# Optimization experiments

Hardware: AMD Instinct MI355X
Metric: run time of the kernel (lower is better)

The kernel has to match this reference:

```python
import jax, jax.numpy as jnp
import numpy as np

N_NODES = 200000
D_IN = 512
HID = 512
D_OUT = 256
B = 1024
SIZES = (25, 10)


def setup_inputs() -> dict:
    key = jax.random.key(0)
    ks = jax.random.split(key, 8)
    x = jax.random.normal(ks[0], (N_NODES, D_IN), dtype=jnp.float32)
    nodes = jax.random.randint(ks[1], (B,), 0, N_NODES)
    neigh1 = jax.random.randint(ks[2], (B * SIZES[0],), 0, N_NODES)
    neigh2 = jax.random.randint(ks[3], (B * SIZES[0] * SIZES[1],), 0, N_NODES)
    # SAGEAggregator weights, stored as [in, out] (torch Linear weight transposed); bias=False
    s = 0.05
    Ws0 = jax.random.normal(ks[4], (D_IN, HID), dtype=jnp.float32) * s
    Wn0 = jax.random.normal(ks[5], (D_IN, HID), dtype=jnp.float32) * s
    Ws1 = jax.random.normal(ks[6], (2 * HID, D_OUT), dtype=jnp.float32) * s
    Wn1 = jax.random.normal(ks[7], (2 * HID, D_OUT), dtype=jnp.float32) * s
    return {"x": x, "nodes": nodes, "neigh1": neigh1, "neigh2": neigh2,
            "Ws0": Ws0, "Wn0": Wn0, "Ws1": Ws1, "Wn1": Wn1}


def _sage_agg(h_self, h_neigh, Ws, Wn, concat):
    # h_self: [M, d], h_neigh: [M, fanout, d] -> mean aggregate then linear transforms
    m = jnp.mean(h_neigh, axis=1)
    a = h_self @ Ws
    b = m @ Wn
    return jnp.concatenate([a, b], axis=-1) if concat else a + b


def reference(x, nodes, neigh1, neigh2, Ws0, Wn0, Ws1, Wn1):
    # gather features for root nodes and sampled 1-hop / 2-hop neighborhoods
    h0 = x[nodes]    # [B, D_IN]
    h1 = x[neigh1]   # [B*25, D_IN]
    h2 = x[neigh2]   # [B*25*10, D_IN]
    d = D_IN
    # layer 0 (concat=True), act=relu, dropout is identity (inference)
    h0 = jax.nn.relu(_sage_agg(h0, h1.reshape(-1, SIZES[0], d), Ws0, Wn0, True))  # [B, 2*HID]
    h1 = jax.nn.relu(_sage_agg(h1, h2.reshape(-1, SIZES[1], d), Ws0, Wn0, True))  # [B*25, 2*HID]
    d2 = 2 * HID
    # layer 1 (last aggregator, concat=False -> sum), no activation
    out = _sage_agg(h0, h1.reshape(-1, SIZES[0], d2), Ws1, Wn1, False)  # [B, D_OUT]
    return out
```

## Files before the change

### kernel.cpp

```cpp
#include <hip/hip_runtime.h>
#include <hip/hip_bf16.h>


#define DEVINL __device__ __forceinline__

typedef __bf16 bf16x8 __attribute__((ext_vector_type(8)));
typedef float f32x4 __attribute__((ext_vector_type(4)));

DEVINL unsigned short f2bf(float f) {
  union { float f; unsigned u; } v; v.f = f;
  unsigned r = v.u + 0x7FFFu + ((v.u >> 16) & 1u);
  return (unsigned short)(r >> 16);
}
DEVINL float bf2f(unsigned short h) {
  union { unsigned u; float f; } v; v.u = ((unsigned)h) << 16;
  return v.f;
}

DEVINL void gload_lds16(const void* g, void* l) {
  __builtin_amdgcn_global_load_lds(
      (const __attribute__((address_space(1))) void*)g,
      (__attribute__((address_space(3))) void*)l, 16, 0, 0);
}

__global__ void weights_cast_kernel(const float* __restrict__ Ws0, const float* __restrict__ Wn0,
                                    const float* __restrict__ Ws1, const float* __restrict__ Wn1,
                                    unsigned short* __restrict__ WT0s, unsigned short* __restrict__ WT0n,
                                    unsigned short* __restrict__ WT1s, unsigned short* __restrict__ WT1n) {
  int t = blockIdx.x * 256 + threadIdx.x;
  int region = t >> 18, local = t & 262143;
  const float* W; unsigned short* WT; int k, n, N;
  if (region == 0)      { W = Ws0; WT = WT0s; }
  else if (region == 1) { W = Wn0; WT = WT0n; }
  else if (region == 2) { W = Ws1; WT = WT1s; }
  else                  { W = Wn1; WT = WT1n; }
  if (region < 2) { k = local & 511;  n = local >> 9;  N = 512; }
  else            { k = local & 1023; n = local >> 10; N = 256; }
  WT[local] = f2bf(W[(size_t)k * N + n]);
}

__global__ void zero_out_kernel(float4* __restrict__ out) {
  out[blockIdx.x * 256 + threadIdx.x] = float4{0.f, 0.f, 0.f, 0.f};
}

__global__ void gather_self_kernel(const float* __restrict__ x,
                                   const int* __restrict__ neigh1,
                                   const int* __restrict__ nodes,
                                   unsigned short* __restrict__ out) {
  int row = blockIdx.x * 2 + (threadIdx.x >> 7);
  int src = row < 25600 ? neigh1[row] : nodes[row - 25600];
  int c4 = (threadIdx.x & 127) << 2;
  const float4 v = *reinterpret_cast<const float4*>(x + (size_t)src * 512 + c4);
  ushort4 o; o.x = f2bf(v.x); o.y = f2bf(v.y); o.z = f2bf(v.z); o.w = f2bf(v.w);
  *reinterpret_cast<ushort4*>(out + (size_t)row * 512 + c4) = o;
}

__global__ void gather_mean10_kernel(const float* __restrict__ x,
                                     const int* __restrict__ idx,
                                     unsigned short* __restrict__ out) {
  int row = blockIdx.x * 2 + (threadIdx.x >> 7);
  int c4 = (threadIdx.x & 127) << 2;
  float4 acc = {0.f, 0.f, 0.f, 0.f};
  const int* ip = idx + (size_t)row * 10;
  #pragma unroll
  for (int j = 0; j < 10; ++j) {
    const float4 v = *reinterpret_cast<const float4*>(x + (size_t)ip[j] * 512 + c4);
    acc.x += v.x; acc.y += v.y; acc.z += v.z; acc.w += v.w;
  }
  const float s = 0.1f;
  ushort4 o; o.x = f2bf(acc.x * s); o.y = f2bf(acc.y * s);
  o.z = f2bf(acc.z * s); o.w = f2bf(acc.w * s);
  *reinterpret_cast<ushort4*>(out + (size_t)row * 512 + c4) = o;
}

template <int COLS>
__global__ void group_mean25_kernel(const unsigned short* __restrict__ in,
                                    unsigned short* __restrict__ out) {
  constexpr int TPG = COLS / 4;
  int g = blockIdx.x * (256 / TPG) + threadIdx.x / TPG;
  int c4 = (threadIdx.x % TPG) * 4;
  float a0 = 0, a1 = 0, a2 = 0, a3 = 0;
  for (int j = 0; j < 25; ++j) {
    ushort4 v = *reinterpret_cast<const ushort4*>(in + ((size_t)g * 25 + j) * COLS + c4);
    a0 += bf2f(v.x); a1 += bf2f(v.y); a2 += bf2f(v.z); a3 += bf2f(v.w);
  }
  const float s = 1.0f / 25.0f;
  ushort4 o; o.x = f2bf(a0 * s); o.y = f2bf(a1 * s); o.z = f2bf(a2 * s); o.w = f2bf(a3 * s);
  *reinterpret_cast<ushort4*>(out + (size_t)g * COLS + c4) = o;
}

template <bool RELU, bool OUTF32, bool ATOMIC>
DEVINL void gemm_core(const unsigned short* __restrict__ A, int lda,
                      const unsigned short* __restrict__ Bt, int ldb,
                      void* __restrict__ C, int ldc, int Kc,
                      long tm, long tn, long col0,
                      unsigned short* As, unsigned short* Bs) {
  const int t = threadIdx.x;
  const int w = t >> 6;
  const int l = t & 63;
  const int wm = w >> 1, wn = w & 1;
  f32x4 acc[4][4] = {};
  const int s_r = l >> 2;
  const int s_kc = (l & 3) * 8;

  for (int kt = 0; kt < Kc; kt += 32) {
    __syncthreads();
    #pragma unroll
    for (int r = 0; r < 2; ++r) {
      const int chunk = r * 64 + w * 16;
      gload_lds16(A + (size_t)(tm + chunk + s_r) * lda + kt + s_kc, As + chunk * 32);
      gload_lds16(Bt + (size_t)(tn + chunk + s_r) * ldb + kt + s_kc, Bs + chunk * 32);
    }
    __syncthreads();

    bf16x8 af[4], bfr[4];
    const unsigned short* Ab = As + ((size_t)(wm * 64 + (l & 15)) * 32 + (l >> 4) * 8);
    const unsigned short* Bb = Bs + ((size_t)(wn * 64 + (l & 15)) * 32 + (l >> 4) * 8);
    #pragma unroll
    for (int f = 0; f < 4; ++f) {
      af[f] = *reinterpret_cast<const bf16x8*>(Ab + f * 16 * 32);
      bfr[f] = *reinterpret_cast<const bf16x8*>(Bb + f * 16 * 32);
    }
    #pragma unroll
    for (int i = 0; i < 4; ++i)
      #pragma unroll
      for (int j = 0; j < 4; ++j)
        acc[i][j] = __builtin_amdgcn_mfma_f32_16x16x32_bf16(af[i], bfr[j], acc[i][j], 0, 0, 0);
  }

  #pragma unroll
  for (int i = 0; i < 4; ++i) {
    #pragma unroll
    for (int j = 0; j < 4; ++j) {
      #pragma unroll
      for (int r = 0; r < 4; ++r) {
        float v = acc[i][j][r];
        if (RELU) v = fmaxf(v, 0.0f);
        const long row = tm + wm * 64 + i * 16 + (l >> 4) * 4 + r;
        const long col = col0 + tn + wn * 64 + j * 16 + (l & 15);
        if (OUTF32) {
          if (ATOMIC) atomicAdd((float*)C + row * ldc + col, v);
          else        ((float*)C)[row * ldc + col] = v;
        } else {
          ((unsigned short*)C)[row * ldc + col] = f2bf(v);
        }
      }
    }
  }
}

__global__ __launch_bounds__(256) void gemm0_kernel(
    const unsigned short* __restrict__ Hall, const unsigned short* __restrict__ Hmall,
    const unsigned short* __restrict__ WT0s, const unsigned short* __restrict__ WT0n,
    unsigned short* __restrict__ C1all) {
  __shared__ __align__(16) unsigned short As[128 * 32];
  __shared__ __align__(16) unsigned short Bs[128 * 32];
  const int half = blockIdx.x >> 2;
  const long tn = (long)(blockIdx.x & 3) * 128;
  const long tm = (long)blockIdx.y * 128;
  gemm_core<true, false, false>(half ? Hmall : Hall, 512,
                                half ? WT0n : WT0s, 512,
                                C1all, 1024, 512, tm, tn, half ? 512 : 0, As, Bs);
}

__global__ __launch_bounds__(256) void gemm1_kernel(
    const unsigned short* __restrict__ C0, const unsigned short* __restrict__ WT1s,
    const unsigned short* __restrict__ M1, const unsigned short* __restrict__ WT1n,
    float* __restrict__ out) {
  __shared__ __align__(16) unsigned short As[128 * 32];
  __shared__ __align__(16) unsigned short Bs[128 * 32];
  const int pass = blockIdx.z >> 2;
  const int k0 = (blockIdx.z & 3) * 256;
  gemm_core<false, true, true>((pass ? M1 : C0) + k0, 1024,
                               (pass ? WT1n : WT1s) + k0, 1024,
                               out, 256, 256,
                               (long)blockIdx.y * 128, (long)blockIdx.x * 128, 0, As, Bs);
}

extern "C" void kernel_launch(void* const* d_in, const int* in_sizes, int n_in,
                              void* d_out, int out_size, void* d_ws, size_t ws_size,
                              hipStream_t stream) {
  const float* x      = (const float*)d_in[0];
  const int*   nodes  = (const int*)d_in[1];
  const int*   neigh1 = (const int*)d_in[2];
  const int*   neigh2 = (const int*)d_in[3];
  const float* Ws0    = (const float*)d_in[4];
  const float* Wn0    = (const float*)d_in[5];
  const float* Ws1    = (const float*)d_in[6];
  const float* Wn1    = (const float*)d_in[7];
  float* out = (float*)d_out;

  char* p = (char*)d_ws;
  unsigned short* WT0s  = (unsigned short*)p; p += (size_t)512 * 512 * 2;
  unsigned short* WT0n  = (unsigned short*)p; p += (size_t)512 * 512 * 2;
  unsigned short* WT1s  = (unsigned short*)p; p += (size_t)256 * 1024 * 2;
  unsigned short* WT1n  = (unsigned short*)p; p += (size_t)256 * 1024 * 2;
  unsigned short* Hall  = (unsigned short*)p; p += (size_t)26624 * 512 * 2;
  unsigned short* Hmall = (unsigned short*)p; p += (size_t)26624 * 512 * 2;
  unsigned short* C1all = (unsigned short*)p; p += (size_t)26624 * 1024 * 2;
  unsigned short* M1    = (unsigned short*)p; p += (size_t)1024 * 1024 * 2;

  unsigned short* H0m = Hmall + (size_t)25600 * 512;
  const unsigned short* C0 = C1all + (size_t)25600 * 1024;

  hipLaunchKernelGGL(weights_cast_kernel, dim3(4096), dim3(256), 0, stream,
                     Ws0, Wn0, Ws1, Wn1, WT0s, WT0n, WT1s, WT1n);
  hipLaunchKernelGGL(zero_out_kernel, dim3(256), dim3(256), 0, stream, (float4*)out);

  hipLaunchKernelGGL(gather_self_kernel, dim3(13312), dim3(256), 0, stream, x, neigh1, nodes, Hall);
  hipLaunchKernelGGL(gather_mean10_kernel, dim3(12800), dim3(256), 0, stream, x, neigh2, Hmall);
  hipLaunchKernelGGL(group_mean25_kernel<512>, dim3(512), dim3(256), 0, stream, Hall, H0m);

  hipLaunchKernelGGL(gemm0_kernel, dim3(8, 208), dim3(256), 0, stream,
                     Hall, Hmall, WT0s, WT0n, C1all);

  hipLaunchKernelGGL(group_mean25_kernel<1024>, dim3(1024), dim3(256), 0, stream, C1all, M1);

  hipLaunchKernelGGL(gemm1_kernel, dim3(2, 8, 8), dim3(256), 0, stream,
                     C0, WT1s, M1, WT1n, out);
}
```

Before: 190.9 us.

## Fuse group-mean into GEMM0 epilogue with atomics and merge kernels into phases

Replaces the materialized 26624x1024 bf16 C1all buffer with an epilogue that sums ReLU outputs of each 25-row group and accumulates them into an fp32 M1 buffer via atomics. Only the root-node rows are stored as bf16. The separate gather, cast, zero and mean kernels are merged into phase kernels, so the self-half GEMM overlaps with the 2-hop gather. The aim is to cut a large intermediate write and re-read plus several launches. In exchange it adds many global float atomics, an extra fp32 scratch buffer and a conversion pass, and the fp32 summation order becomes nondeterministic.

```diff
diff --git a/kernel.cpp b/kernel.cpp
--- a/kernel.cpp
+++ b/kernel.cpp
@@ -23,77 +23,12 @@
       (__attribute__((address_space(3))) void*)l, 16, 0, 0);
 }
 
-__global__ void weights_cast_kernel(const float* __restrict__ Ws0, const float* __restrict__ Wn0,
-                                    const float* __restrict__ Ws1, const float* __restrict__ Wn1,
-                                    unsigned short* __restrict__ WT0s, unsigned short* __restrict__ WT0n,
-                                    unsigned short* __restrict__ WT1s, unsigned short* __restrict__ WT1n) {
-  int t = blockIdx.x * 256 + threadIdx.x;
-  int region = t >> 18, local = t & 262143;
-  const float* W; unsigned short* WT; int k, n, N;
-  if (region == 0)      { W = Ws0; WT = WT0s; }
-  else if (region == 1) { W = Wn0; WT = WT0n; }
-  else if (region == 2) { W = Ws1; WT = WT1s; }
-  else                  { W = Wn1; WT = WT1n; }
-  if (region < 2) { k = local & 511;  n = local >> 9;  N = 512; }
-  else            { k = local & 1023; n = local >> 10; N = 256; }
-  WT[local] = f2bf(W[(size_t)k * N + n]);
-}
-
-__global__ void zero_out_kernel(float4* __restrict__ out) {
-  out[blockIdx.x * 256 + threadIdx.x] = float4{0.f, 0.f, 0.f, 0.f};
-}
-
-__global__ void gather_self_kernel(const float* __restrict__ x,
-                                   const int* __restrict__ neigh1,
-                                   const int* __restrict__ nodes,
-                                   unsigned short* __restrict__ out) {
-  int row = blockIdx.x * 2 + (threadIdx.x >> 7);
-  int src = row < 25600 ? neigh1[row] : nodes[row - 25600];
-  int c4 = (threadIdx.x & 127) << 2;
-  const float4 v = *reinterpret_cast<const float4*>(x + (size_t)src * 512 + c4);
-  ushort4 o; o.x = f2bf(v.x); o.y = f2bf(v.y); o.z = f2bf(v.z); o.w = f2bf(v.w);
-  *reinterpret_cast<ushort4*>(out + (size_t)row * 512 + c4) = o;
-}
-
-__global__ void gather_mean10_kernel(const float* __restrict__ x,
-                                     const int* __restrict__ idx,
-                                     unsigned short* __restrict__ out) {
-  int row = blockIdx.x * 2 + (threadIdx.x >> 7);
-  int c4 = (threadIdx.x & 127) << 2;
-  float4 acc = {0.f, 0.f, 0.f, 0.f};
-  const int* ip = idx + (size_t)row * 10;
-  #pragma unroll
-  for (int j = 0; j < 10; ++j) {
-    const float4 v = *reinterpret_cast<const float4*>(x + (size_t)ip[j] * 512 + c4);
-    acc.x += v.x; acc.y += v.y; acc.z += v.z; acc.w += v.w;
-  }
-  const float s = 0.1f;
-  ushort4 o; o.x = f2bf(acc.x * s); o.y = f2bf(acc.y * s);
-  o.z = f2bf(acc.z * s); o.w = f2bf(acc.w * s);
-  *reinterpret_cast<ushort4*>(out + (size_t)row * 512 + c4) = o;
-}
-
-template <int COLS>
-__global__ void group_mean25_kernel(const unsigned short* __restrict__ in,
-                                    unsigned short* __restrict__ out) {
-  constexpr int TPG = COLS / 4;
-  int g = blockIdx.x * (256 / TPG) + threadIdx.x / TPG;
-  int c4 = (threadIdx.x % TPG) * 4;
-  float a0 = 0, a1 = 0, a2 = 0, a3 = 0;
-  for (int j = 0; j < 25; ++j) {
-    ushort4 v = *reinterpret_cast<const ushort4*>(in + ((size_t)g * 25 + j) * COLS + c4);
-    a0 += bf2f(v.x); a1 += bf2f(v.y); a2 += bf2f(v.z); a3 += bf2f(v.w);
-  }
-  const float s = 1.0f / 25.0f;
-  ushort4 o; o.x = f2bf(a0 * s); o.y = f2bf(a1 * s); o.z = f2bf(a2 * s); o.w = f2bf(a3 * s);
-  *reinterpret_cast<ushort4*>(out + (size_t)g * COLS + c4) = o;
-}
-
-template <bool RELU, bool OUTF32, bool ATOMIC>
+template <int EPI>
 DEVINL void gemm_core(const unsigned short* __restrict__ A, int lda,
                       const unsigned short* __restrict__ Bt, int ldb,
-                      void* __restrict__ C, int ldc, int Kc,
-                      long tm, long tn, long col0,
+                      int Kc, long tm, long tn, int col0,
+                      unsigned short* __restrict__ C0, float* __restrict__ M1f,
+                      float* __restrict__ out, int ldc,
                       unsigned short* As, unsigned short* Bs) {
   const int t = threadIdx.x;
   const int w = t >> 6;
@@ -128,42 +63,157 @@
         acc[i][j] = __builtin_amdgcn_mfma_f32_16x16x32_bf16(af[i], bfr[j], acc[i][j], 0, 0, 0);
   }
 
-  #pragma unroll
-  for (int i = 0; i < 4; ++i) {
-    #pragma unroll
-    for (int j = 0; j < 4; ++j) {
-      #pragma unroll
-      for (int r = 0; r < 4; ++r) {
-        float v = acc[i][j][r];
-        if (RELU) v = fmaxf(v, 0.0f);
-        const long row = tm + wm * 64 + i * 16 + (l >> 4) * 4 + r;
-        const long col = col0 + tn + wn * 64 + j * 16 + (l & 15);
-        if (OUTF32) {
-          if (ATOMIC) atomicAdd((float*)C + row * ldc + col, v);
-          else        ((float*)C)[row * ldc + col] = v;
-        } else {
-          ((unsigned short*)C)[row * ldc + col] = f2bf(v);
+  const int q = l >> 4, cl = l & 15;
+  if (EPI == 0) {
+    if (tm < 25600) {
+      #pragma unroll
+      for (int i = 0; i < 4; ++i) {
+        const int base = (int)tm + wm * 64 + i * 16 + q * 4;
+        const int g = base / 25;
+        const int rem = base - g * 25;
+        #pragma unroll
+        for (int j = 0; j < 4; ++j) {
+          const int col = col0 + (int)tn + wn * 64 + j * 16 + cl;
+          float v0 = fmaxf(acc[i][j][0], 0.f), v1 = fmaxf(acc[i][j][1], 0.f);
+          float v2 = fmaxf(acc[i][j][2], 0.f), v3 = fmaxf(acc[i][j][3], 0.f);
+          if (rem <= 21) {
+            atomicAdd(M1f + (size_t)g * 1024 + col, v0 + v1 + v2 + v3);
+          } else {
+            const int s = 25 - rem;
+            float a = v0, b = 0.f;
+            if (s > 1) a += v1; else b += v1;
+            if (s > 2) a += v2; else b += v2;
+            b += v3;
+            atomicAdd(M1f + (size_t)g * 1024 + col, a);
+            atomicAdd(M1f + (size_t)(g + 1) * 1024 + col, b);
+          }
         }
       }
-    }
-  }
-}
-
-__global__ __launch_bounds__(256) void gemm0_kernel(
-    const unsigned short* __restrict__ Hall, const unsigned short* __restrict__ Hmall,
-    const unsigned short* __restrict__ WT0s, const unsigned short* __restrict__ WT0n,
-    unsigned short* __restrict__ C1all) {
+    } else {
+      #pragma unroll
+      for (int i = 0; i < 4; ++i)
+        #pragma unroll
+        for (int j = 0; j < 4; ++j)
+          #pragma unroll
+          for (int r = 0; r < 4; ++r) {
+            const long row = tm - 25600 + wm * 64 + i * 16 + q * 4 + r;
+            const long col = col0 + tn + wn * 64 + j * 16 + cl;
+            C0[row * 1024 + col] = f2bf(fmaxf(acc[i][j][r], 0.f));
+          }
+    }
+  } else {
+    #pragma unroll
+    for (int i = 0; i < 4; ++i)
+      #pragma unroll
+      for (int j = 0; j < 4; ++j)
+        #pragma unroll
+        for (int r = 0; r < 4; ++r) {
+          const long row = tm + wm * 64 + i * 16 + q * 4 + r;
+          const long col = tn + wn * 64 + j * 16 + cl;
+          atomicAdd(out + row * ldc + col, acc[i][j][r]);
+        }
+  }
+}
+
+__global__ __launch_bounds__(256) void phase0_kernel(
+    const float* __restrict__ x, const int* __restrict__ neigh1, const int* __restrict__ nodes,
+    const float* __restrict__ Ws0, const float* __restrict__ Wn0,
+    const float* __restrict__ Ws1, const float* __restrict__ Wn1,
+    unsigned short* __restrict__ Hall,
+    unsigned short* __restrict__ WT0s, unsigned short* __restrict__ WT0n,
+    unsigned short* __restrict__ WT1s, unsigned short* __restrict__ WT1n,
+    float* __restrict__ M1f, float* __restrict__ out) {
+  const int b = blockIdx.x;
+  const int tid = threadIdx.x;
+  if (b < 13312) {
+    int row = b * 2 + (tid >> 7);
+    int src = row < 25600 ? neigh1[row] : nodes[row - 25600];
+    int c4 = (tid & 127) << 2;
+    const float4 v = *reinterpret_cast<const float4*>(x + (size_t)src * 512 + c4);
+    ushort4 o; o.x = f2bf(v.x); o.y = f2bf(v.y); o.z = f2bf(v.z); o.w = f2bf(v.w);
+    *reinterpret_cast<ushort4*>(Hall + (size_t)row * 512 + c4) = o;
+  } else if (b < 13312 + 4096) {
+    int t = (b - 13312) * 256 + tid;
+    int region = t >> 18, local = t & 262143;
+    const float* W; unsigned short* WT;
+    if (region == 0)      { W = Ws0; WT = WT0s; }
+    else if (region == 1) { W = Wn0; WT = WT0n; }
+    else if (region == 2) { W = Ws1; WT = WT1s; }
+    else                  { W = Wn1; WT = WT1n; }
+    int k, n, N;
+    if (region < 2) { k = local & 511;  n = local >> 9;  N = 512; }
+    else            { k = local & 1023; n = local >> 10; N = 256; }
+    WT[local] = f2bf(W[(size_t)k * N + n]);
+  } else if (b < 13312 + 4096 + 1024) {
+    int t = (b - 17408) * 256 + tid;
+    reinterpret_cast<float4*>(M1f)[t] = float4{0.f, 0.f, 0.f, 0.f};
+  } else {
+    int t = (b - 18432) * 256 + tid;
+    reinterpret_cast<float4*>(out)[t] = float4{0.f, 0.f, 0.f, 0.f};
+  }
+}
+
+__global__ __launch_bounds__(256) void phase1_kernel(
+    const float* __restrict__ x, const int* __restrict__ neigh2,
+    const unsigned short* __restrict__ Hall, const unsigned short* __restrict__ WT0s,
+    unsigned short* __restrict__ Hmall,
+    unsigned short* __restrict__ C0, float* __restrict__ M1f) {
   __shared__ __align__(16) unsigned short As[128 * 32];
   __shared__ __align__(16) unsigned short Bs[128 * 32];
-  const int half = blockIdx.x >> 2;
+  const int b = blockIdx.x;
+  const int tid = threadIdx.x;
+  if (b < 832) {
+    const long tm = (long)(b >> 2) * 128;
+    const long tn = (long)(b & 3) * 128;
+    gemm_core<0>(Hall, 512, WT0s, 512, 512, tm, tn, 0, C0, M1f, nullptr, 0, As, Bs);
+  } else if (b < 832 + 12800) {
+    int row = (b - 832) * 2 + (tid >> 7);
+    int c4 = (tid & 127) << 2;
+    float4 acc = {0.f, 0.f, 0.f, 0.f};
+    const int* ip = neigh2 + (size_t)row * 10;
+    #pragma unroll
+    for (int j = 0; j < 10; ++j) {
+      const float4 v = *reinterpret_cast<const float4*>(x + (size_t)ip[j] * 512 + c4);
+      acc.x += v.x; acc.y += v.y; acc.z += v.z; acc.w += v.w;
+    }
+    const float s = 0.1f;
+    ushort4 o; o.x = f2bf(acc.x * s); o.y = f2bf(acc.y * s);
+    o.z = f2bf(acc.z * s); o.w = f2bf(acc.w * s);
+    *reinterpret_cast<ushort4*>(Hmall + (size_t)row * 512 + c4) = o;
+  } else {
+    int g = (b - 13632) * 2 + (tid >> 7);
+    int c4 = (tid & 127) << 2;
+    float a0 = 0, a1 = 0, a2 = 0, a3 = 0;
+    for (int j = 0; j < 25; ++j) {
+      ushort4 v = *reinterpret_cast<const ushort4*>(Hall + ((size_t)g * 25 + j) * 512 + c4);
+      a0 += bf2f(v.x); a1 += bf2f(v.y); a2 += bf2f(v.z); a3 += bf2f(v.w);
+    }
+    const float s = 1.0f / 25.0f;
+    ushort4 o; o.x = f2bf(a0 * s); o.y = f2bf(a1 * s); o.z = f2bf(a2 * s); o.w = f2bf(a3 * s);
+    *reinterpret_cast<ushort4*>(Hmall + ((size_t)25600 + g) * 512 + c4) = o;
+  }
+}
+
+__global__ __launch_bounds__(256) void phase2_kernel(
+    const unsigned short* __restrict__ Hmall, const unsigned short* __restrict__ WT0n,
+    unsigned short* __restrict__ C0, float* __restrict__ M1f) {
+  __shared__ __align__(16) unsigned short As[128 * 32];
+  __shared__ __align__(16) unsigned short Bs[128 * 32];
+  const long tm = (long)(blockIdx.x >> 2) * 128;
   const long tn = (long)(blockIdx.x & 3) * 128;
-  const long tm = (long)blockIdx.y * 128;
-  gemm_core<true, false, false>(half ? Hmall : Hall, 512,
-                                half ? WT0n : WT0s, 512,
-                                C1all, 1024, 512, tm, tn, half ? 512 : 0, As, Bs);
-}
-
-__global__ __launch_bounds__(256) void gemm1_kernel(
+  gemm_core<0>(Hmall, 512, WT0n, 512, 512, tm, tn, 512, C0, M1f, nullptr, 0, As, Bs);
+}
+
+__global__ __launch_bounds__(256) void phase3_kernel(const float* __restrict__ M1f,
+                                                     unsigned short* __restrict__ M1) {
+  int t = blockIdx.x * 256 + threadIdx.x;
+  const float4 v = reinterpret_cast<const float4*>(M1f)[t];
+  const float s = 1.0f / 25.0f;
+  ushort4 o; o.x = f2bf(v.x * s); o.y = f2bf(v.y * s); o.z = f2bf(v.z * s); o.w = f2bf(v.w * s);
+  reinterpret_cast<ushort4*>(M1)[t] = o;
+}
+
+__global__ __launch_bounds__(256) void phase4_kernel(
     const unsigned short* __restrict__ C0, const unsigned short* __restrict__ WT1s,
     const unsigned short* __restrict__ M1, const unsigned short* __restrict__ WT1n,
     float* __restrict__ out) {
@@ -171,10 +221,9 @@
   __shared__ __align__(16) unsigned short Bs[128 * 32];
   const int pass = blockIdx.z >> 2;
   const int k0 = (blockIdx.z & 3) * 256;
-  gemm_core<false, true, true>((pass ? M1 : C0) + k0, 1024,
-                               (pass ? WT1n : WT1s) + k0, 1024,
-                               out, 256, 256,
-                               (long)blockIdx.y * 128, (long)blockIdx.x * 128, 0, As, Bs);
+  gemm_core<1>((pass ? M1 : C0) + k0, 1024, (pass ? WT1n : WT1s) + k0, 1024, 256,
+               (long)blockIdx.y * 128, (long)blockIdx.x * 128, 0,
+               nullptr, nullptr, out, 256, As, Bs);
 }
 
 extern "C" void kernel_launch(void* const* d_in, const int* in_sizes, int n_in,
@@ -197,25 +246,18 @@
   unsigned short* WT1n  = (unsigned short*)p; p += (size_t)256 * 1024 * 2;
   unsigned short* Hall  = (unsigned short*)p; p += (size_t)26624 * 512 * 2;
   unsigned short* Hmall = (unsigned short*)p; p += (size_t)26624 * 512 * 2;
-  unsigned short* C1all = (unsigned short*)p; p += (size_t)26624 * 1024 * 2;
+  unsigned short* C0    = (unsigned short*)p; p += (size_t)1024 * 1024 * 2;
   unsigned short* M1    = (unsigned short*)p; p += (size_t)1024 * 1024 * 2;
-
-  unsigned short* H0m = Hmall + (size_t)25600 * 512;
-  const unsigned short* C0 = C1all + (size_t)25600 * 1024;
-
-  hipLaunchKernelGGL(weights_cast_kernel, dim3(4096), dim3(256), 0, stream,
-                     Ws0, Wn0, Ws1, Wn1, WT0s, WT0n, WT1s, WT1n);
-  hipLaunchKernelGGL(zero_out_kernel, dim3(256), dim3(256), 0, stream, (float4*)out);
-
-  hipLaunchKernelGGL(gather_self_kernel, dim3(13312), dim3(256), 0, stream, x, neigh1, nodes, Hall);
-  hipLaunchKernelGGL(gather_mean10_kernel, dim3(12800), dim3(256), 0, stream, x, neigh2, Hmall);
-  hipLaunchKernelGGL(group_mean25_kernel<512>, dim3(512), dim3(256), 0, stream, Hall, H0m);
-
-  hipLaunchKernelGGL(gemm0_kernel, dim3(8, 208), dim3(256), 0, stream,
-                     Hall, Hmall, WT0s, WT0n, C1all);
-
-  hipLaunchKernelGGL(group_mean25_kernel<1024>, dim3(1024), dim3(256), 0, stream, C1all, M1);
-
-  hipLaunchKernelGGL(gemm1_kernel, dim3(2, 8, 8), dim3(256), 0, stream,
+  float*          M1f   = (float*)p;          p += (size_t)1024 * 1024 * 4;
+
+  hipLaunchKernelGGL(phase0_kernel, dim3(18688), dim3(256), 0, stream,
+                     x, neigh1, nodes, Ws0, Wn0, Ws1, Wn1,
+                     Hall, WT0s, WT0n, WT1s, WT1n, M1f, out);
+  hipLaunchKernelGGL(phase1_kernel, dim3(14144), dim3(256), 0, stream,
+                     x, neigh2, Hall, WT0s, Hmall, C0, M1f);
+  hipLaunchKernelGGL(phase2_kernel, dim3(832), dim3(256), 0, stream,
+                     Hmall, WT0n, C0, M1f);
+  hipLaunchKernelGGL(phase3_kernel, dim3(1024), dim3(256), 0, stream, M1f, M1);
+  hipLaunchKernelGGL(phase4_kernel, dim3(2, 8, 8), dim3(256), 0, stream,
                      C0, WT1s, M1, WT1n, out);
 }
```

New measurement: 215.1 us. +12.6%, slower.
